# Optimization experiments

Hardware: AMD Instinct MI355X
Metric: run time of the kernel (lower is better)

## Reference

```python
import jax, jax.numpy as jnp
import numpy as np

B, C, H, W, N, NH, DFF = 2, 256, 128, 128, 8, 8, 1024
EPS = 1e-5


def _ln(x, g, b):
    m = jnp.mean(x, -1, keepdims=True)
    v = jnp.mean((x - m) ** 2, -1, keepdims=True)
    return (x - m) / jnp.sqrt(v + EPS) * g + b


def _mha(q, k, v, Wqkv, bqkv, Wo, bo, nh):
    # q,k,v: [Bq, S, C]; torch MultiheadAttention with packed in_proj
    Bq, S, Cd = q.shape
    dh = Cd // nh
    Wq, Wk, Wv = jnp.split(Wqkv, 3, axis=0)
    bq, bk, bv = jnp.split(bqkv, 3, axis=0)
    qp = (q @ Wq.T + bq).reshape(Bq, S, nh, dh).transpose(0, 2, 1, 3)
    kp = (k @ Wk.T + bk).reshape(Bq, S, nh, dh).transpose(0, 2, 1, 3)
    vp = (v @ Wv.T + bv).reshape(Bq, S, nh, dh).transpose(0, 2, 1, 3)
    scores = jnp.einsum('bhqd,bhkd->bhqk', qp, kp) / jnp.sqrt(jnp.asarray(dh, qp.dtype))
    attn = jax.nn.softmax(scores, axis=-1)
    o = jnp.einsum('bhqk,bhkd->bhqd', attn, vp).transpose(0, 2, 1, 3).reshape(Bq, S, Cd)
    return o @ Wo.T + bo


def _enc_layer(q, k, v, Wqkv, bqkv, Wo, bo, W1, b1, W2, b2, g1, be1, g2, be2, nh):
    # normalize_before=False, dropout=0
    src = _ln(v + _mha(q, k, v, Wqkv, bqkv, Wo, bo, nh), g1, be1)
    ffn = jax.nn.relu(src @ W1.T + b1) @ W2.T + b2
    return _ln(src + ffn, g2, be2)


def _encode(feat, pe, layer_params, nh):
    # feat: [Nv, hw, C]; pe = glob_pos + rel_pos broadcast: [Nv, hw, C]
    out = feat
    qk = out + pe
    out = _enc_layer(qk, qk, out, *layer_params, nh)
    out_t = out.transpose(1, 0, 2)                 # [hw, Nv, C] axis-permuted pass
    qk = out_t + pe.transpose(1, 0, 2)
    out = _enc_layer(qk, qk, out_t, *layer_params, nh).transpose(1, 0, 2)
    return out


def _forward(backbone_memory, defe_feature_filtered, glob_pos_embed,
             Wqkv, bqkv, Wo, bo, W1, b1, W2, b2, g1, be1, g2, be2,
             relW1, relb1, relW2, relb2, n):
    Bm, Cd, Hf, Wf = backbone_memory.shape
    h, w = Hf // n, Wf // n
    Nv, hw = n * n, h * w

    # relative position embedding: MLP over normalized grid coords [h,w,2]
    gy, gx = jnp.meshgrid(jnp.arange(h, dtype=jnp.float32),
                          jnp.arange(w, dtype=jnp.float32), indexing='ij')
    coords = jnp.stack([gx / (w - 1), gy / (h - 1)], axis=-1)
    rel = (jax.nn.relu(coords @ relW1.T + relb1) @ relW2.T + relb2)  # [h,w,C]
    rel = rel.reshape(1, hw, Cd)                                      # [1,hw,C]

    # window partition: [B, Nv, hw, C]
    win = backbone_memory.reshape(Bm, Cd, n, h, n, w).transpose(0, 2, 4, 1, 3, 5)
    win = win.reshape(Bm, Nv, Cd, hw).transpose(0, 1, 3, 2)

    # per-window global pos embed: [Nv, hw, C]
    glob = glob_pos_embed.reshape(Cd, n, h, n, w).transpose(1, 3, 0, 2, 4)
    glob = glob.reshape(Nv, Cd, hw).transpose(0, 2, 1)

    pe = glob + rel
    layer_params = (Wqkv, bqkv, Wo, bo, W1, b1, W2, b2, g1, be1, g2, be2)
    enc = jax.vmap(lambda f: _encode(f, pe, layer_params, NH))(win)   # [B,Nv,hw,C]

    # scatter windows back and add residually (reconstructed += feats)
    back = enc.transpose(0, 1, 3, 2).reshape(Bm, n, n, Cd, h, w)
    back = back.transpose(0, 3, 1, 4, 2, 5).reshape(Bm, Cd, Hf, Wf)
    reconstructed = backbone_memory + back

    # defe_mask via non-overlapping max-pool (all-ones mask -> all valid)
    Hm, Wm = defe_feature_filtered.shape[-2:]
    kh = (Hm // Hf) * h
    kw = (Wm // Wf) * w
    pooled = defe_feature_filtered.reshape(Bm, 1, n, kh, n, kw).max(axis=(3, 5))
    defe_mask = pooled[:, 0] > 0
    return reconstructed, defe_mask


def setup_inputs() -> dict:
    key = jax.random.key(0)
    ks = jax.random.split(key, 10)
    s = 0.02
    return {
        'backbone_memory': jax.random.normal(ks[0], (B, C, H, W), jnp.float32),
        'defe_feature_filtered': jnp.ones((B, 1, H, W), jnp.float32),
        'glob_pos_embed': jax.random.normal(ks[1], (C, H, W), jnp.float32),
        'Wqkv': jax.random.normal(ks[2], (3 * C, C), jnp.float32) * s,
        'bqkv': jnp.zeros((3 * C,), jnp.float32),
        'Wo': jax.random.normal(ks[3], (C, C), jnp.float32) * s,
        'bo': jnp.zeros((C,), jnp.float32),
        'W1': jax.random.normal(ks[4], (DFF, C), jnp.float32) * s,
        'b1': jnp.zeros((DFF,), jnp.float32),
        'W2': jax.random.normal(ks[5], (C, DFF), jnp.float32) * s,
        'b2': jnp.zeros((C,), jnp.float32),
        'g1': jnp.ones((C,), jnp.float32),
        'be1': jnp.zeros((C,), jnp.float32),
        'g2': jnp.ones((C,), jnp.float32),
        'be2': jnp.zeros((C,), jnp.float32),
        'relW1': jax.random.normal(ks[6], (64, 2), jnp.float32) * s,
        'relb1': jnp.zeros((64,), jnp.float32),
        'relW2': jax.random.normal(ks[7], (C, 64), jnp.float32) * s,
        'relb2': jnp.zeros((C,), jnp.float32),
        'n': N,
    }


def reference(backbone_memory, defe_feature_filtered, glob_pos_embed,
              Wqkv, bqkv, Wo, bo, W1, b1, W2, b2, g1, be1, g2, be2,
              relW1, relb1, relW2, relb2, n):
    return _forward(backbone_memory, defe_feature_filtered, glob_pos_embed,
                    Wqkv, bqkv, Wo, bo, W1, b1, W2, b2, g1, be1, g2, be2,
                    relW1, relb1, relW2, relb2, n)
```

## Files before the change

### kernel.cpp

```cpp
#include <hip/hip_runtime.h>
#include <hip/hip_bf16.h>

#define C_DIM 256
#define NHEAD 8
#define DH 32
#define NTOK 32768
#define PETOK 16384
#define DFF_DIM 1024
#define LN_EPS 1e-5f

typedef unsigned int u32;
typedef unsigned short ushortT;
using frag_ab = __attribute__((ext_vector_type(8))) short;
using f32x4   = __attribute__((ext_vector_type(4))) float;

__device__ __forceinline__ float bflo(u32 u) { union { u32 i; float f; } c; c.i = u << 16; return c.f; }
__device__ __forceinline__ float bfhi(u32 u) { union { u32 i; float f; } c; c.i = u & 0xffff0000u; return c.f; }
__device__ __forceinline__ float b2f(ushortT u) { union { u32 i; float f; } c; c.i = ((u32)u) << 16; return c.f; }
__device__ __forceinline__ ushortT f2b(float f) {
    __hip_bfloat16 b = __float2bfloat16(f);
    return *reinterpret_cast<ushortT*>(&b);
}
__device__ __forceinline__ u32 packbf(float lo, float hi) {
    return (u32)f2b(lo) | ((u32)f2b(hi) << 16);
}
__device__ __forceinline__ void gload_lds16(const ushortT* g, ushortT* l) {
    __builtin_amdgcn_global_load_lds((const __attribute__((address_space(1))) void*)g,
                                     (__attribute__((address_space(3))) void*)l, 16, 0, 0);
}

__global__ void cvt_all_kernel(const float* __restrict__ Wqkv, const float* __restrict__ Wo,
                               const float* __restrict__ W1, const float* __restrict__ W2,
                               ushortT* __restrict__ dst) {
    const int i = (blockIdx.x * 256 + threadIdx.x) * 4;
    const float* src;
    int off;
    if (i < 196608)      { src = Wqkv; off = 0; }
    else if (i < 262144) { src = Wo;   off = 196608; }
    else if (i < 524288) { src = W1;   off = 262144; }
    else                 { src = W2;   off = 524288; }
    const float4 v = *(const float4*)&src[i - off];
    uint2 o = {packbf(v.x, v.y), packbf(v.z, v.w)};
    *(uint2*)&dst[i] = o;
}

__global__ void rel_kernel(const float* __restrict__ relW1, const float* __restrict__ relb1,
                           const float* __restrict__ relW2, const float* __restrict__ relb2,
                           float* __restrict__ rel) {
    __shared__ float hid[64];
    int t = blockIdx.x;
    int ty = t >> 4, tx = t & 15;
    float cx = tx * (1.0f / 15.0f);
    float cy = ty * (1.0f / 15.0f);
    int c = threadIdx.x;
    if (c < 64) {
        float h = relW1[c * 2 + 0] * cx + relW1[c * 2 + 1] * cy + relb1[c];
        hid[c] = fmaxf(h, 0.0f);
    }
    __syncthreads();
    float acc = relb2[c];
    #pragma unroll
    for (int jj = 0; jj < 64; ++jj) acc = fmaf(hid[jj], relW2[c * 64 + jj], acc);
    rel[t * C_DIM + c] = acc;
}

__global__ __launch_bounds__(256) void pe_kernel(const float* __restrict__ glob,
                                                 const float* __restrict__ rel,
                                                 ushortT* __restrict__ peb) {
    __shared__ float tile[32][129];
    const int y = blockIdx.x;
    const int c0 = blockIdx.y * 32;
    const int i = y >> 4, ty = y & 15;
    const int tid = threadIdx.x;
    const int xl = tid & 127;
    #pragma unroll
    for (int p = 0; p < 16; ++p) {
        const int cl = p * 2 + (tid >> 7);
        tile[cl][xl] = glob[(size_t)(c0 + cl) * 16384 + y * 128 + xl];
    }
    __syncthreads();
    const int cl = tid & 31;
    #pragma unroll
    for (int p = 0; p < 16; ++p) {
        const int x = p * 8 + (tid >> 5);
        const int v = i * 8 + (x >> 4);
        const int t = ty * 16 + (x & 15);
        const float val = tile[cl][x] + rel[t * C_DIM + c0 + cl];
        peb[(size_t)(v * 256 + t) * C_DIM + c0 + cl] = f2b(val);
    }
}

__global__ __launch_bounds__(256) void window_kernel(const float* __restrict__ backbone,
                                                     ushortT* __restrict__ Xb) {
    __shared__ float tile[32][129];
    const int y = blockIdx.x;
    const int c0 = blockIdx.y * 32;
    const int b = blockIdx.z;
    const int i = y >> 4, ty = y & 15;
    const int tid = threadIdx.x;
    const int xl = tid & 127;
    #pragma unroll
    for (int p = 0; p < 16; ++p) {
        const int cl = p * 2 + (tid >> 7);
        tile[cl][xl] = backbone[(size_t)b * 4194304 + (size_t)(c0 + cl) * 16384 + y * 128 + xl];
    }
    __syncthreads();
    const int cl = tid & 31;
    #pragma unroll
    for (int p = 0; p < 16; ++p) {
        const int x = p * 8 + (tid >> 5);
        const int v = i * 8 + (x >> 4);
        const int t = ty * 16 + (x & 15);
        const size_t tok = (size_t)b * PETOK + v * 256 + t;
        Xb[tok * C_DIM + c0 + cl] = f2b(tile[cl][x]);
    }
}

__global__ __launch_bounds__(256) void scatter_kernel(const float* __restrict__ backbone,
                                                      const ushortT* __restrict__ X,
                                                      float* __restrict__ out) {
    __shared__ ushortT tile[128][34];
    const int y = blockIdx.x;
    const int c0 = blockIdx.y * 32;
    const int b = blockIdx.z;
    const int i = y >> 4, ty = y & 15;
    const int tid = threadIdx.x;
    const int cl = tid & 31;
    #pragma unroll
    for (int p = 0; p < 16; ++p) {
        const int x = p * 8 + (tid >> 5);
        const int v = i * 8 + (x >> 4);
        const int t = ty * 16 + (x & 15);
        const size_t tok = (size_t)b * PETOK + v * 256 + t;
        tile[x][cl] = X[tok * C_DIM + c0 + cl];
    }
    __syncthreads();
    const int xl = tid & 127;
    #pragma unroll
    for (int p = 0; p < 16; ++p) {
        const int c = c0 + p * 2 + (tid >> 7);
        const size_t gi = (size_t)b * 4194304 + (size_t)c * 16384 + y * 128 + xl;
        out[gi] = backbone[gi] + b2f(tile[xl][p * 2 + (tid >> 7)]);
    }
}

#define BM 128
#define BN 128
#define BK 32

template<bool FUSE_PE, bool RELU>
__global__ __launch_bounds__(256) void gemm_bf16(
        const ushortT* __restrict__ A, int lda,
        const ushortT* __restrict__ peb,
        const ushortT* __restrict__ W,
        const float* __restrict__ bias,
        ushortT* __restrict__ Cout, int ldc, int K) {
    __shared__ ushortT As[BM][BK];
    __shared__ ushortT Bs[BN][BK];
    const int nwg = gridDim.x * gridDim.y;
    const int flat = blockIdx.y * gridDim.x + blockIdx.x;
    const int cpx = nwg >> 3;
    const int swz = (flat & 7) * cpx + (flat >> 3);
    const int m0 = (swz / gridDim.x) * BM;
    const int n0 = (swz % gridDim.x) * BN;
    const int tid = threadIdx.x;
    const int lane = tid & 63;
    const int wave = tid >> 6;
    const int wm = (wave >> 1) * 64;
    const int wn = (wave & 1) * 64;
    const int fr = lane & 15;
    const int fg = lane >> 4;
    const int gRow = wave * 32 + (lane >> 2);
    const int gCol = (lane & 3) * 8;
    const int sRow = tid >> 2;
    const int sCol = (tid & 3) * 8;

    f32x4 acc[4][4];
    #pragma unroll
    for (int i = 0; i < 4; ++i)
        #pragma unroll
        for (int j = 0; j < 4; ++j)
            acc[i][j] = (f32x4){0.f, 0.f, 0.f, 0.f};

    for (int k0 = 0; k0 < K; k0 += BK) {
        if (FUSE_PE) {
            #pragma unroll
            for (int h = 0; h < 2; ++h) {
                const int row = sRow + h * 64;
                uint4 av = *(const uint4*)&A[(size_t)(m0 + row) * lda + k0 + sCol];
                const uint4 pv = *(const uint4*)&peb[(size_t)((m0 + row) & 16383) * C_DIM + k0 + sCol];
                u32* a = (u32*)&av;
                const u32* p = (const u32*)&pv;
                #pragma unroll
                for (int e = 0; e < 4; ++e)
                    a[e] = packbf(bflo(a[e]) + bflo(p[e]), bfhi(a[e]) + bfhi(p[e]));
                *(uint4*)&As[row][sCol] = av;
            }
        } else {
            gload_lds16(&A[(size_t)(m0 + gRow) * lda + k0 + gCol], &As[wave * 32][0]);
            gload_lds16(&A[(size_t)(m0 + gRow + 16) * lda + k0 + gCol], &As[wave * 32 + 16][0]);
        }
        gload_lds16(&W[(size_t)(n0 + gRow) * K + k0 + gCol], &Bs[wave * 32][0]);
        gload_lds16(&W[(size_t)(n0 + gRow + 16) * K + k0 + gCol], &Bs[wave * 32 + 16][0]);
        __syncthreads();
        frag_ab af[4], bf[4];
        #pragma unroll
        for (int i = 0; i < 4; ++i) af[i] = *(const frag_ab*)&As[wm + i * 16 + fr][fg * 8];
        #pragma unroll
        for (int j = 0; j < 4; ++j) bf[j] = *(const frag_ab*)&Bs[wn + j * 16 + fr][fg * 8];
        #pragma unroll
        for (int i = 0; i < 4; ++i)
            #pragma unroll
            for (int j = 0; j < 4; ++j)
                acc[i][j] = __builtin_amdgcn_mfma_f32_16x16x32_bf16(af[i], bf[j], acc[i][j], 0, 0, 0);
        __syncthreads();
    }
    #pragma unroll
    for (int j = 0; j < 4; ++j) {
        const float bv = bias[n0 + wn + j * 16 + fr];
        #pragma unroll
        for (int i = 0; i < 4; ++i) {
            #pragma unroll
            for (int r = 0; r < 4; ++r) {
                float v = acc[i][j][r] + bv;
                if (RELU) v = fmaxf(v, 0.0f);
                const int m = m0 + wm + i * 16 + fg * 4 + r;
                const int n = n0 + wn + j * 16 + fr;
                Cout[(size_t)m * ldc + n] = f2b(v);
            }
        }
    }
}

__global__ __launch_bounds__(512) void gemm_ln(
        const ushortT* __restrict__ A,
        const ushortT* __restrict__ W,
        const float* __restrict__ bias,
        const float* __restrict__ g, const float* __restrict__ be,
        ushortT* __restrict__ Xr, int K) {
    __shared__ ushortT smem[64 * 264];
    ushortT* As = smem;
    ushortT* Bs = smem + 2048;
    const int m0 = blockIdx.x * 64;
    const int tid = threadIdx.x;
    const int lane = tid & 63;
    const int wave = tid >> 6;
    const int wm = (wave >> 2) * 32;
    const int wn = (wave & 3) * 64;
    const int fr = lane & 15;
    const int fg = lane >> 4;
    const int gR = lane >> 2;
    const int gC = (lane & 3) * 8;

    f32x4 acc[2][4];
    #pragma unroll
    for (int i = 0; i < 2; ++i)
        #pragma unroll
        for (int j = 0; j < 4; ++j)
            acc[i][j] = (f32x4){0.f, 0.f, 0.f, 0.f};

    for (int k0 = 0; k0 < K; k0 += BK) {
        if (wave < 4)
            gload_lds16(&A[(size_t)(m0 + wave * 16 + gR) * K + k0 + gC], &As[wave * 16 * 32]);
        gload_lds16(&W[(size_t)(wave * 32 + gR) * K + k0 + gC], &Bs[wave * 32 * 32]);
        gload_lds16(&W[(size_t)(wave * 32 + 16 + gR) * K + k0 + gC], &Bs[(wave * 32 + 16) * 32]);
        __syncthreads();
        frag_ab af[2], bf[4];
        #pragma unroll
        for (int i = 0; i < 2; ++i) af[i] = *(const frag_ab*)&As[(wm + i * 16 + fr) * 32 + fg * 8];
        #pragma unroll
        for (int j = 0; j < 4; ++j) bf[j] = *(const frag_ab*)&Bs[(wn + j * 16 + fr) * 32 + fg * 8];
        #pragma unroll
        for (int i = 0; i < 2; ++i)
            #pragma unroll
            for (int j = 0; j < 4; ++j)
                acc[i][j] = __builtin_amdgcn_mfma_f32_16x16x32_bf16(af[i], bf[j], acc[i][j], 0, 0, 0);
        __syncthreads();
    }
    ushortT* Yl = smem;
    #pragma unroll
    for (int j = 0; j < 4; ++j) {
        const int n = wn + j * 16 + fr;
        const float bv = bias[n];
        #pragma unroll
        for (int i = 0; i < 2; ++i)
            #pragma unroll
            for (int r = 0; r < 4; ++r)
                Yl[(wm + i * 16 + fg * 4 + r) * 264 + n] = f2b(acc[i][j][r] + bv);
    }
    __syncthreads();
    const int row = tid >> 3;
    const int part = tid & 7;
    const size_t tok = (size_t)(m0 + row);
    float vv[4][8];
    float s = 0.f, ss = 0.f;
    #pragma unroll
    for (int q = 0; q < 4; ++q) {
        const uint4 yu = *(const uint4*)&Yl[row * 264 + part * 32 + q * 8];
        const uint4 xu = *(const uint4*)&Xr[tok * C_DIM + part * 32 + q * 8];
        const u32 yw[4] = {yu.x, yu.y, yu.z, yu.w};
        const u32 xw[4] = {xu.x, xu.y, xu.z, xu.w};
        #pragma unroll
        for (int e = 0; e < 4; ++e) {
            const float a = bflo(yw[e]) + bflo(xw[e]);
            const float b = bfhi(yw[e]) + bfhi(xw[e]);
            vv[q][2 * e] = a;
            vv[q][2 * e + 1] = b;
            s += a + b;
            ss += a * a + b * b;
        }
    }
    #pragma unroll
    for (int off = 1; off <= 4; off <<= 1) {
        s += __shfl_xor(s, off, 64);
        ss += __shfl_xor(ss, off, 64);
    }
    const float mean = s * (1.0f / 256.0f);
    const float var = ss * (1.0f / 256.0f) - mean * mean;
    const float inv = rsqrtf(var + LN_EPS);
    #pragma unroll
    for (int q = 0; q < 4; ++q) {
        const float4 ga = *(const float4*)&g[part * 32 + q * 8];
        const float4 gb = *(const float4*)&g[part * 32 + q * 8 + 4];
        const float4 ba = *(const float4*)&be[part * 32 + q * 8];
        const float4 bb = *(const float4*)&be[part * 32 + q * 8 + 4];
        const float o0 = (vv[q][0] - mean) * inv * ga.x + ba.x;
        const float o1 = (vv[q][1] - mean) * inv * ga.y + ba.y;
        const float o2 = (vv[q][2] - mean) * inv * ga.z + ba.z;
        const float o3 = (vv[q][3] - mean) * inv * ga.w + ba.w;
        const float o4 = (vv[q][4] - mean) * inv * gb.x + bb.x;
        const float o5 = (vv[q][5] - mean) * inv * gb.y + bb.y;
        const float o6 = (vv[q][6] - mean) * inv * gb.z + bb.z;
        const float o7 = (vv[q][7] - mean) * inv * gb.w + bb.w;
        uint4 ou;
        ou.x = packbf(o0, o1);
        ou.y = packbf(o2, o3);
        ou.z = packbf(o4, o5);
        ou.w = packbf(o6, o7);
        *(uint4*)&Xr[tok * C_DIM + part * 32 + q * 8] = ou;
    }
}

#define KVC 128
__global__ __launch_bounds__(256) void attn_p0(const ushortT* __restrict__ QKb,
                                               const ushortT* __restrict__ Vb,
                                               ushortT* __restrict__ Ob) {
    __shared__ ushortT K_lds[KVC * 40];
    __shared__ ushortT V_t[32 * 136];
    __shared__ ushortT P_lds[4][16 * 136];
    const int grp = blockIdx.x;
    const int h = grp & 7;
    const int bv = grp >> 3;
    const int base = (bv >> 6) * PETOK + (bv & 63) * 256;
    const int tid = threadIdx.x;
    const int wave = tid >> 6;
    const int lane = tid & 63;
    const int fr = lane & 15;
    const int fg = lane >> 4;
    const float scale = 0.17677669529663687f;

    frag_ab qf[4];
    size_t qtok[4];
    #pragma unroll
    for (int s = 0; s < 4; ++s) {
        qtok[s] = (size_t)(base + wave * 64 + s * 16 + fr);
        qf[s] = *(const frag_ab*)&QKb[qtok[s] * 512 + h * DH + fg * 8];
    }
    float m[4], l[4];
    f32x4 o0[4], o1[4];
    #pragma unroll
    for (int s = 0; s < 4; ++s) {
        m[s] = -1e30f; l[s] = 0.f;
        o0[s] = (f32x4){0.f, 0.f, 0.f, 0.f};
        o1[s] = (f32x4){0.f, 0.f, 0.f, 0.f};
    }

    for (int c = 0; c < 2; ++c) {
        __syncthreads();
        #pragma unroll
        for (int it = 0; it < 2; ++it) {
            const int idx = it * 256 + tid;
            const int row = idx >> 2, ch = idx & 3;
            const size_t tok = (size_t)(base + c * KVC + row);
            const uint4 kv = *(const uint4*)&QKb[tok * 512 + 256 + h * DH + ch * 8];
            *(uint4*)&K_lds[row * 40 + ch * 8] = kv;
            const uint4 vv = *(const uint4*)&Vb[tok * C_DIM + h * DH + ch * 8];
            const ushortT* vp = (const ushortT*)&vv;
            #pragma unroll
            for (int e = 0; e < 8; ++e) V_t[(ch * 8 + e) * 136 + row] = vp[e];
        }
        __syncthreads();
        #pragma unroll
        for (int s = 0; s < 4; ++s) {
            f32x4 sc[8];
            #pragma unroll
            for (int kt = 0; kt < 8; ++kt) {
                const frag_ab kf = *(const frag_ab*)&K_lds[(kt * 16 + fr) * 40 + fg * 8];
                sc[kt] = __builtin_amdgcn_mfma_f32_16x16x32_bf16(kf, qf[s], (f32x4){0.f, 0.f, 0.f, 0.f}, 0, 0, 0);
            }
            float mx = -1e30f;
            #pragma unroll
            for (int kt = 0; kt < 8; ++kt)
                mx = fmaxf(mx, fmaxf(fmaxf(sc[kt][0], sc[kt][1]), fmaxf(sc[kt][2], sc[kt][3])));
            mx = fmaxf(mx, __shfl_xor(mx, 16, 64));
            mx = fmaxf(mx, __shfl_xor(mx, 32, 64));
            const float nm = fmaxf(m[s], mx);
            const float corr = __expf((m[s] - nm) * scale);
            m[s] = nm;
            float lsum = 0.f;
            #pragma unroll
            for (int kt = 0; kt < 8; ++kt) {
                const float p0 = __expf((sc[kt][0] - nm) * scale);
                const float p1 = __expf((sc[kt][1] - nm) * scale);
                const float p2 = __expf((sc[kt][2] - nm) * scale);
                const float p3 = __expf((sc[kt][3] - nm) * scale);
                lsum += (p0 + p1) + (p2 + p3);
                uint2 pk;
                pk.x = packbf(p0, p1);
                pk.y = packbf(p2, p3);
                *(uint2*)&P_lds[wave][fr * 136 + kt * 16 + fg * 4] = pk;
            }
            lsum += __shfl_xor(lsum, 16, 64);
            lsum += __shfl_xor(lsum, 32, 64);
            l[s] = l[s] * corr + lsum;
            o0[s] *= corr;
            o1[s] *= corr;
            #pragma unroll
            for (int kc = 0; kc < 4; ++kc) {
                const frag_ab pf = *(const frag_ab*)&P_lds[wave][fr * 136 + kc * 32 + fg * 8];
                const frag_ab v0 = *(const frag_ab*)&V_t[fr * 136 + kc * 32 + fg * 8];
                const frag_ab v1 = *(const frag_ab*)&V_t[(16 + fr) * 136 + kc * 32 + fg * 8];
                o0[s] = __builtin_amdgcn_mfma_f32_16x16x32_bf16(v0, pf, o0[s], 0, 0, 0);
                o1[s] = __builtin_amdgcn_mfma_f32_16x16x32_bf16(v1, pf, o1[s], 0, 0, 0);
            }
        }
    }
    #pragma unroll
    for (int s = 0; s < 4; ++s) {
        const float inv = 1.0f / l[s];
        ushortT* ob = &Ob[qtok[s] * C_DIM + h * DH];
        uint2 w0, w1;
        w0.x = packbf(o0[s][0] * inv, o0[s][1] * inv);
        w0.y = packbf(o0[s][2] * inv, o0[s][3] * inv);
        w1.x = packbf(o1[s][0] * inv, o1[s][1] * inv);
        w1.y = packbf(o1[s][2] * inv, o1[s][3] * inv);
        *(uint2*)&ob[fg * 4] = w0;
        *(uint2*)&ob[16 + fg * 4] = w1;
    }
}

__global__ __launch_bounds__(256) void attn_p1(const ushortT* __restrict__ QKb,
                                               const ushortT* __restrict__ Vb,
                                               ushortT* __restrict__ Ob) {
    __shared__ ushortT K_lds[4][64 * 40];
    __shared__ ushortT V_t[4][32 * 72];
    __shared__ ushortT P_lds[4][16 * 72];
    const int wave = threadIdx.x >> 6;
    const int lane = threadIdx.x & 63;
    const int unit = blockIdx.x * 4 + wave;
    const int h = unit & 7;
    const int g = unit >> 3;
    const int base = (g >> 8) * PETOK + (g & 255);
    const int fr = lane & 15;
    const int fg = lane >> 4;
    const float scale = 0.17677669529663687f;
    #pragma unroll
    for (int it = 0; it < 4; ++it) {
        const int idx = it * 64 + lane;
        const int row = idx >> 2, ch = idx & 3;
        const size_t tok = (size_t)(base + row * 256);
        const uint4 kv = *(const uint4*)&QKb[tok * 512 + 256 + h * DH + ch * 8];
        *(uint4*)&K_lds[wave][row * 40 + ch * 8] = kv;
        const uint4 vv = *(const uint4*)&Vb[tok * C_DIM + h * DH + ch * 8];
        const ushortT* vp = (const ushortT*)&vv;
        #pragma unroll
        for (int e = 0; e < 8; ++e) V_t[wave][(ch * 8 + e) * 72 + row] = vp[e];
    }
    #pragma unroll
    for (int s = 0; s < 4; ++s) {
        const int qq = s * 16 + fr;
        const size_t qtok = (size_t)(base + qq * 256);
        const frag_ab qf = *(const frag_ab*)&QKb[qtok * 512 + h * DH + fg * 8];
        f32x4 sc[4];
        #pragma unroll
        for (int kt = 0; kt < 4; ++kt) {
            const frag_ab kf = *(const frag_ab*)&K_lds[wave][(kt * 16 + fr) * 40 + fg * 8];
            sc[kt] = __builtin_amdgcn_mfma_f32_16x16x32_bf16(kf, qf, (f32x4){0.f, 0.f, 0.f, 0.f}, 0, 0, 0);
        }
        float mx = -1e30f;
        #pragma unroll
        for (int kt = 0; kt < 4; ++kt)
            mx = fmaxf(mx, fmaxf(fmaxf(sc[kt][0], sc[kt][1]), fmaxf(sc[kt][2], sc[kt][3])));
        mx = fmaxf(mx, __shfl_xor(mx, 16, 64));
        mx = fmaxf(mx, __shfl_xor(mx, 32, 64));
        float lsum = 0.f;
        #pragma unroll
        for (int kt = 0; kt < 4; ++kt) {
            const float p0 = __expf((sc[kt][0] - mx) * scale);
            const float p1 = __expf((sc[kt][1] - mx) * scale);
            const float p2 = __expf((sc[kt][2] - mx) * scale);
            const float p3 = __expf((sc[kt][3] - mx) * scale);
            lsum += (p0 + p1) + (p2 + p3);
            uint2 pk;
            pk.x = packbf(p0, p1);
            pk.y = packbf(p2, p3);
            *(uint2*)&P_lds[wave][fr * 72 + kt * 16 + fg * 4] = pk;
        }
        lsum += __shfl_xor(lsum, 16, 64);
        lsum += __shfl_xor(lsum, 32, 64);
        f32x4 o0 = {0.f, 0.f, 0.f, 0.f}, o1 = {0.f, 0.f, 0.f, 0.f};
        #pragma unroll
        for (int kc = 0; kc < 2; ++kc) {
            const frag_ab pf = *(const frag_ab*)&P_lds[wave][fr * 72 + kc * 32 + fg * 8];
            const frag_ab v0 = *(const frag_ab*)&V_t[wave][fr * 72 + kc * 32 + fg * 8];
            const frag_ab v1 = *(const frag_ab*)&V_t[wave][(16 + fr) * 72 + kc * 32 + fg * 8];
            o0 = __builtin_amdgcn_mfma_f32_16x16x32_bf16(v0, pf, o0, 0, 0, 0);
            o1 = __builtin_amdgcn_mfma_f32_16x16x32_bf16(v1, pf, o1, 0, 0, 0);
        }
        const float inv = 1.0f / lsum;
        ushortT* ob = &Ob[qtok * C_DIM + h * DH];
        uint2 w0, w1;
        w0.x = packbf(o0[0] * inv, o0[1] * inv);
        w0.y = packbf(o0[2] * inv, o0[3] * inv);
        w1.x = packbf(o1[0] * inv, o1[1] * inv);
        w1.y = packbf(o1[2] * inv, o1[3] * inv);
        *(uint2*)&ob[fg * 4] = w0;
        *(uint2*)&ob[16 + fg * 4] = w1;
    }
}

__global__ void mask_kernel(const float* __restrict__ defe, float* __restrict__ out) {
    __shared__ float wmax[4];
    const int idx = blockIdx.x;
    const int b = idx >> 6;
    const int ii = (idx >> 3) & 7;
    const int jj = idx & 7;
    const int t = threadIdx.x;
    const int y = t >> 4, xx = t & 15;
    float v = defe[b * 16384 + (ii * 16 + y) * 128 + jj * 16 + xx];
    #pragma unroll
    for (int off = 32; off; off >>= 1) v = fmaxf(v, __shfl_xor(v, off, 64));
    if ((t & 63) == 0) wmax[t >> 6] = v;
    __syncthreads();
    if (t == 0) {
        float mx = fmaxf(fmaxf(wmax[0], wmax[1]), fmaxf(wmax[2], wmax[3]));
        out[8388608 + idx] = (mx > 0.0f) ? 1.0f : 0.0f;
    }
}

extern "C" void kernel_launch(void* const* d_in, const int* in_sizes, int n_in,
                              void* d_out, int out_size, void* d_ws, size_t ws_size,
                              hipStream_t stream) {
    const float* backbone = (const float*)d_in[0];
    const float* defe     = (const float*)d_in[1];
    const float* glob     = (const float*)d_in[2];
    const float* Wqkv     = (const float*)d_in[3];
    const float* bqkv     = (const float*)d_in[4];
    const float* Wo       = (const float*)d_in[5];
    const float* bo       = (const float*)d_in[6];
    const float* W1       = (const float*)d_in[7];
    const float* b1       = (const float*)d_in[8];
    const float* W2       = (const float*)d_in[9];
    const float* b2       = (const float*)d_in[10];
    const float* g1       = (const float*)d_in[11];
    const float* be1      = (const float*)d_in[12];
    const float* g2       = (const float*)d_in[13];
    const float* be2      = (const float*)d_in[14];
    const float* relW1    = (const float*)d_in[15];
    const float* relb1    = (const float*)d_in[16];
    const float* relW2    = (const float*)d_in[17];
    const float* relb2    = (const float*)d_in[18];

    ushortT* peb    = (ushortT*)d_ws;
    ushortT* Wqkv_b = peb + 4194304;
    ushortT* Wo_b   = Wqkv_b + 196608;
    ushortT* W1_b   = Wo_b + 65536;
    ushortT* W2_b   = W1_b + 262144;
    ushortT* Xb     = W2_b + 262144;
    ushortT* QKb    = Xb + 8388608;
    ushortT* Vb     = QKb + 16777216;
    ushortT* Ob     = Vb + 8388608;
    ushortT* Hb     = QKb;
    float*   relf   = (float*)(Ob + 8388608);
    size_t needed = (size_t)((char*)(relf + 65536) - (char*)d_ws);
    if (ws_size < needed) return;

    cvt_all_kernel<<<768, 256, 0, stream>>>(Wqkv, Wo, W1, W2, Wqkv_b);
    rel_kernel<<<256, 256, 0, stream>>>(relW1, relb1, relW2, relb2, relf);
    pe_kernel<<<dim3(128, 8), 256, 0, stream>>>(glob, relf, peb);
    window_kernel<<<dim3(128, 8, 2), 256, 0, stream>>>(backbone, Xb);

    for (int pass = 0; pass < 2; ++pass) {
        gemm_bf16<true, false><<<dim3(512 / BN, NTOK / BM), 256, 0, stream>>>(
            Xb, C_DIM, peb, Wqkv_b, bqkv, QKb, 512, C_DIM);
        gemm_bf16<false, false><<<dim3(256 / BN, NTOK / BM), 256, 0, stream>>>(
            Xb, C_DIM, nullptr, Wqkv_b + 512 * 256, bqkv + 512, Vb, C_DIM, C_DIM);
        if (pass == 0) {
            attn_p0<<<128 * NHEAD, 256, 0, stream>>>(QKb, Vb, Ob);
        } else {
            attn_p1<<<4096 / 4, 256, 0, stream>>>(QKb, Vb, Ob);
        }
        gemm_ln<<<NTOK / 64, 512, 0, stream>>>(Ob, Wo_b, bo, g1, be1, Xb, C_DIM);
        gemm_bf16<false, true><<<dim3(DFF_DIM / BN, NTOK / BM), 256, 0, stream>>>(
            Xb, C_DIM, nullptr, W1_b, b1, Hb, DFF_DIM, C_DIM);
        gemm_ln<<<NTOK / 64, 512, 0, stream>>>(Hb, W2_b, b2, g2, be2, Xb, DFF_DIM);
    }

    scatter_kernel<<<dim3(128, 8, 2), 256, 0, stream>>>(backbone, Xb, (float*)d_out);
    mask_kernel<<<128, 256, 0, stream>>>(defe, (float*)d_out);
}
```

Before: 354.8 us.

## Enlarge gemm_ln row tile and compute LayerNorm directly from MFMA accumulators

The fused GEMM+LayerNorm kernel now processes 128 rows per block instead of 64, with each wave holding a 4x4 MFMA accumulator tile. This halves the number of W reloads per token. The epilogue no longer stages a bf16 copy of the output in LDS. It adds the residual in registers, reduces row sums with shuffles plus a small LDS partial-sum table, and writes normalized values directly. This removes a bf16 rounding step and an LDS round trip, but the residual reads and output writes become scattered 2-byte accesses, and register pressure is higher.

```diff
diff --git a/kernel.cpp b/kernel.cpp
--- a/kernel.cpp
+++ b/kernel.cpp
@@ -238,107 +238,103 @@
         const float* __restrict__ bias,
         const float* __restrict__ g, const float* __restrict__ be,
         ushortT* __restrict__ Xr, int K) {
-    __shared__ ushortT smem[64 * 264];
-    ushortT* As = smem;
-    ushortT* Bs = smem + 2048;
-    const int m0 = blockIdx.x * 64;
+    __shared__ ushortT As[128 * 32];
+    __shared__ ushortT Bs[256 * 32];
+    __shared__ float2 part[128][4];
+    const int m0 = blockIdx.x * 128;
     const int tid = threadIdx.x;
     const int lane = tid & 63;
     const int wave = tid >> 6;
-    const int wm = (wave >> 2) * 32;
+    const int wm = (wave >> 2) * 64;
     const int wn = (wave & 3) * 64;
     const int fr = lane & 15;
     const int fg = lane >> 4;
     const int gR = lane >> 2;
     const int gC = (lane & 3) * 8;
 
-    f32x4 acc[2][4];
-    #pragma unroll
-    for (int i = 0; i < 2; ++i)
+    f32x4 acc[4][4];
+    #pragma unroll
+    for (int i = 0; i < 4; ++i)
         #pragma unroll
         for (int j = 0; j < 4; ++j)
             acc[i][j] = (f32x4){0.f, 0.f, 0.f, 0.f};
 
     for (int k0 = 0; k0 < K; k0 += BK) {
-        if (wave < 4)
-            gload_lds16(&A[(size_t)(m0 + wave * 16 + gR) * K + k0 + gC], &As[wave * 16 * 32]);
-        gload_lds16(&W[(size_t)(wave * 32 + gR) * K + k0 + gC], &Bs[wave * 32 * 32]);
+        if (wave < 4) {
+            gload_lds16(&A[(size_t)(m0 + wave * 32 + gR) * K + k0 + gC], &As[(wave * 32) * 32]);
+            gload_lds16(&A[(size_t)(m0 + wave * 32 + 16 + gR) * K + k0 + gC], &As[(wave * 32 + 16) * 32]);
+        }
+        gload_lds16(&W[(size_t)(wave * 32 + gR) * K + k0 + gC], &Bs[(wave * 32) * 32]);
         gload_lds16(&W[(size_t)(wave * 32 + 16 + gR) * K + k0 + gC], &Bs[(wave * 32 + 16) * 32]);
         __syncthreads();
-        frag_ab af[2], bf[4];
-        #pragma unroll
-        for (int i = 0; i < 2; ++i) af[i] = *(const frag_ab*)&As[(wm + i * 16 + fr) * 32 + fg * 8];
+        frag_ab af[4], bf[4];
+        #pragma unroll
+        for (int i = 0; i < 4; ++i) af[i] = *(const frag_ab*)&As[(wm + i * 16 + fr) * 32 + fg * 8];
         #pragma unroll
         for (int j = 0; j < 4; ++j) bf[j] = *(const frag_ab*)&Bs[(wn + j * 16 + fr) * 32 + fg * 8];
         #pragma unroll
-        for (int i = 0; i < 2; ++i)
+        for (int i = 0; i < 4; ++i)
             #pragma unroll
             for (int j = 0; j < 4; ++j)
                 acc[i][j] = __builtin_amdgcn_mfma_f32_16x16x32_bf16(af[i], bf[j], acc[i][j], 0, 0, 0);
         __syncthreads();
     }
-    ushortT* Yl = smem;
+    float bv[4], gv[4], bev[4];
     #pragma unroll
     for (int j = 0; j < 4; ++j) {
         const int n = wn + j * 16 + fr;
-        const float bv = bias[n];
-        #pragma unroll
-        for (int i = 0; i < 2; ++i)
-            #pragma unroll
-            for (int r = 0; r < 4; ++r)
-                Yl[(wm + i * 16 + fg * 4 + r) * 264 + n] = f2b(acc[i][j][r] + bv);
-    }
+        bv[j] = bias[n];
+        gv[j] = g[n];
+        bev[j] = be[n];
+    }
+    #pragma unroll
+    for (int i = 0; i < 4; ++i)
+        #pragma unroll
+        for (int r = 0; r < 4; ++r) {
+            const size_t row = (size_t)(m0 + wm + i * 16 + fg * 4 + r);
+            #pragma unroll
+            for (int j = 0; j < 4; ++j)
+                acc[i][j][r] += bv[j] + b2f(Xr[row * C_DIM + wn + j * 16 + fr]);
+        }
+    #pragma unroll
+    for (int i = 0; i < 4; ++i)
+        #pragma unroll
+        for (int r = 0; r < 4; ++r) {
+            float s = acc[i][0][r] + acc[i][1][r] + acc[i][2][r] + acc[i][3][r];
+            float ss = acc[i][0][r] * acc[i][0][r] + acc[i][1][r] * acc[i][1][r]
+                     + acc[i][2][r] * acc[i][2][r] + acc[i][3][r] * acc[i][3][r];
+            #pragma unroll
+            for (int off = 1; off <= 8; off <<= 1) {
+                s += __shfl_xor(s, off, 64);
+                ss += __shfl_xor(ss, off, 64);
+            }
+            if (fr == 0) {
+                float2 p = {s, ss};
+                part[wm + i * 16 + fg * 4 + r][wave & 3] = p;
+            }
+        }
     __syncthreads();
-    const int row = tid >> 3;
-    const int part = tid & 7;
-    const size_t tok = (size_t)(m0 + row);
-    float vv[4][8];
-    float s = 0.f, ss = 0.f;
-    #pragma unroll
-    for (int q = 0; q < 4; ++q) {
-        const uint4 yu = *(const uint4*)&Yl[row * 264 + part * 32 + q * 8];
-        const uint4 xu = *(const uint4*)&Xr[tok * C_DIM + part * 32 + q * 8];
-        const u32 yw[4] = {yu.x, yu.y, yu.z, yu.w};
-        const u32 xw[4] = {xu.x, xu.y, xu.z, xu.w};
-        #pragma unroll
-        for (int e = 0; e < 4; ++e) {
-            const float a = bflo(yw[e]) + bflo(xw[e]);
-            const float b = bfhi(yw[e]) + bfhi(xw[e]);
-            vv[q][2 * e] = a;
-            vv[q][2 * e + 1] = b;
-            s += a + b;
-            ss += a * a + b * b;
-        }
-    }
-    #pragma unroll
-    for (int off = 1; off <= 4; off <<= 1) {
-        s += __shfl_xor(s, off, 64);
-        ss += __shfl_xor(ss, off, 64);
-    }
-    const float mean = s * (1.0f / 256.0f);
-    const float var = ss * (1.0f / 256.0f) - mean * mean;
-    const float inv = rsqrtf(var + LN_EPS);
-    #pragma unroll
-    for (int q = 0; q < 4; ++q) {
-        const float4 ga = *(const float4*)&g[part * 32 + q * 8];
-        const float4 gb = *(const float4*)&g[part * 32 + q * 8 + 4];
-        const float4 ba = *(const float4*)&be[part * 32 + q * 8];
-        const float4 bb = *(const float4*)&be[part * 32 + q * 8 + 4];
-        const float o0 = (vv[q][0] - mean) * inv * ga.x + ba.x;
-        const float o1 = (vv[q][1] - mean) * inv * ga.y + ba.y;
-        const float o2 = (vv[q][2] - mean) * inv * ga.z + ba.z;
-        const float o3 = (vv[q][3] - mean) * inv * ga.w + ba.w;
-        const float o4 = (vv[q][4] - mean) * inv * gb.x + bb.x;
-        const float o5 = (vv[q][5] - mean) * inv * gb.y + bb.y;
-        const float o6 = (vv[q][6] - mean) * inv * gb.z + bb.z;
-        const float o7 = (vv[q][7] - mean) * inv * gb.w + bb.w;
-        uint4 ou;
-        ou.x = packbf(o0, o1);
-        ou.y = packbf(o2, o3);
-        ou.z = packbf(o4, o5);
-        ou.w = packbf(o6, o7);
-        *(uint4*)&Xr[tok * C_DIM + part * 32 + q * 8] = ou;
-    }
+    #pragma unroll
+    for (int i = 0; i < 4; ++i)
+        #pragma unroll
+        for (int r = 0; r < 4; ++r) {
+            const int row = wm + i * 16 + fg * 4 + r;
+            const float2 p0 = part[row][0];
+            const float2 p1 = part[row][1];
+            const float2 p2 = part[row][2];
+            const float2 p3 = part[row][3];
+            const float s = (p0.x + p1.x) + (p2.x + p3.x);
+            const float ss = (p0.y + p1.y) + (p2.y + p3.y);
+            const float mean = s * (1.0f / 256.0f);
+            const float var = ss * (1.0f / 256.0f) - mean * mean;
+            const float inv = rsqrtf(var + LN_EPS);
+            const size_t gr = (size_t)(m0 + row);
+            #pragma unroll
+            for (int j = 0; j < 4; ++j) {
+                const float o = (acc[i][j][r] - mean) * inv * gv[j] + bev[j];
+                Xr[gr * C_DIM + wn + j * 16 + fr] = f2b(o);
+            }
+        }
 }
 
 #define KVC 128
@@ -600,10 +596,10 @@
         } else {
             attn_p1<<<4096 / 4, 256, 0, stream>>>(QKb, Vb, Ob);
         }
-        gemm_ln<<<NTOK / 64, 512, 0, stream>>>(Ob, Wo_b, bo, g1, be1, Xb, C_DIM);
+        gemm_ln<<<NTOK / 128, 512, 0, stream>>>(Ob, Wo_b, bo, g1, be1, Xb, C_DIM);
         gemm_bf16<false, true><<<dim3(DFF_DIM / BN, NTOK / BM), 256, 0, stream>>>(
             Xb, C_DIM, nullptr, W1_b, b1, Hb, DFF_DIM, C_DIM);
-        gemm_ln<<<NTOK / 64, 512, 0, stream>>>(Hb, W2_b, b2, g2, be2, Xb, DFF_DIM);
+        gemm_ln<<<NTOK / 128, 512, 0, stream>>>(Hb, W2_b, b2, g2, be2, Xb, DFF_DIM);
     }
 
     scatter_kernel<<<dim3(128, 8, 2), 256, 0, stream>>>(backbone, Xb, (float*)d_out);
```

Measured after the change: 359.3 us. No clear change (+1.3%).
